# Kernel optimization log

Hardware: AMD Instinct MI355X
Metric: run time of the kernel (lower is better)

The kernel has to match this reference:

```python
import jax, jax.numpy as jnp
import numpy as np

B, T, C, H = 32, 1024, 384, 64

def setup_inputs() -> dict:
    key = jax.random.key(0)
    k1, k2, k3, k4 = jax.random.split(key, 4)
    x = jax.random.normal(k1, (B, T, C), dtype=jnp.float32)
    s = 1.0 / np.sqrt(C)
    Wk = jax.random.normal(k2, (C, H), dtype=jnp.float32) * s
    Wq = jax.random.normal(k3, (C, H), dtype=jnp.float32) * s
    Wv = jax.random.normal(k4, (C, H), dtype=jnp.float32) * s
    return {"x": x, "Wk": Wk, "Wq": Wq, "Wv": Wv}

def reference(x, Wk, Wq, Wv):
    # Single-head causal attention (dropout = identity, eval mode).
    Tn = x.shape[1]
    k = jnp.einsum('btc,ch->bth', x, Wk)   # [B,T,H]
    q = jnp.einsum('btc,ch->bth', x, Wq)
    v = jnp.einsum('btc,ch->bth', x, Wv)
    scale = k.shape[-1] ** -0.5
    wei = jnp.einsum('bth,bsh->bts', q, k) * scale  # [B,T,T]
    causal = jnp.tril(jnp.ones((Tn, Tn), dtype=bool))
    wei = jnp.where(causal, wei, -jnp.inf)
    wei = jax.nn.softmax(wei, axis=-1)
    out = jnp.einsum('bts,bsh->bth', wei, v)  # [B,T,H]
    return out
```

## Files before the change

kernel.cpp:

```cpp
#include <hip/hip_runtime.h>

#define BB 32
#define TT 1024
#define CCH 384
#define HH 64

typedef short short8 __attribute__((ext_vector_type(8)));
typedef float f32x4 __attribute__((ext_vector_type(4)));
typedef unsigned short ushort;

static __device__ __forceinline__ ushort f2bf(float f) {
    union { float f; unsigned u; } v; v.f = f;
    unsigned r = v.u + 0x7fff + ((v.u >> 16) & 1);
    return (ushort)(r >> 16);
}

__global__ void wswz(const float* __restrict__ Wk, const float* __restrict__ Wq,
                     const float* __restrict__ Wv, ushort* __restrict__ wf) {
    const int mat = blockIdx.x, ks = blockIdx.y;
    const float* W = (mat == 0) ? Wk : ((mat == 1) ? Wq : Wv);
    const int t = threadIdx.x;
    const int ct = t >> 6, lane = t & 63, quad = lane >> 4, l15 = lane & 15;
    const int col = ct * 16 + l15;
    short8 d;
#pragma unroll
    for (int j = 0; j < 8; ++j)
        d[j] = (short)f2bf(W[(ks * 32 + quad * 8 + j) * 64 + col]);
    *(short8*)(wf + (((mat * 12 + ks) * 4 + ct) << 9) + lane * 8) = d;
}

#define XSTR 388
#define VS_STRIDE 68

__global__ __launch_bounds__(256, 2) void qkv(const float* __restrict__ x,
                                              const ushort* __restrict__ wf,
                                              ushort* __restrict__ kb,
                                              ushort* __restrict__ qb,
                                              ushort* __restrict__ vtb) {
    const int r0 = blockIdx.x * 64;
    const int tid = threadIdx.x;
    const int wv = tid >> 6, lane = tid & 63, l15 = lane & 15, quad = lane >> 4;

    __shared__ ushort xs[64 * XSTR];

#pragma unroll
    for (int kb3 = 0; kb3 < 3; ++kb3) {
        const int kbase = kb3 * 128;
        const int seg = (tid & 7) * 16;
#pragma unroll
        for (int i = 0; i < 2; ++i) {
            const int r = (tid >> 3) + 32 * i;
            const float* src = x + (size_t)(r0 + r) * CCH + kbase + seg;
            f32x4 v0 = *(const f32x4*)(src);
            f32x4 v1 = *(const f32x4*)(src + 4);
            f32x4 v2 = *(const f32x4*)(src + 8);
            f32x4 v3 = *(const f32x4*)(src + 12);
            short8 p0, p1;
#pragma unroll
            for (int j = 0; j < 4; ++j) {
                p0[j]     = (short)f2bf(v0[j]);
                p0[j + 4] = (short)f2bf(v1[j]);
                p1[j]     = (short)f2bf(v2[j]);
                p1[j + 4] = (short)f2bf(v3[j]);
            }
            *(short8*)(xs + r * XSTR + kbase + seg) = p0;
            *(short8*)(xs + r * XSTR + kbase + seg + 8) = p1;
        }
    }
    __syncthreads();

    f32x4 acc[12] = {};
    short8 bf[2][12];
#pragma unroll
    for (int m = 0; m < 3; ++m)
#pragma unroll
        for (int ct = 0; ct < 4; ++ct)
            bf[0][m * 4 + ct] = *(const short8*)(wf + (((m * 12 + 0) * 4 + ct) << 9) + lane * 8);

#pragma unroll
    for (int ks = 0; ks < 12; ++ks) {
        short8 a = *(const short8*)(xs + (wv * 16 + l15) * XSTR + ks * 32 + quad * 8);
        if (ks < 11) {
#pragma unroll
            for (int m = 0; m < 3; ++m)
#pragma unroll
                for (int ct = 0; ct < 4; ++ct)
                    bf[(ks + 1) & 1][m * 4 + ct] =
                        *(const short8*)(wf + (((m * 12 + ks + 1) * 4 + ct) << 9) + lane * 8);
        }
#pragma unroll
        for (int f = 0; f < 12; ++f)
            acc[f] = __builtin_amdgcn_mfma_f32_16x16x32_bf16(a, bf[ks & 1][f], acc[f], 0, 0, 0);
    }

#pragma unroll
    for (int ct = 0; ct < 4; ++ct) {
#pragma unroll
        for (int r = 0; r < 4; ++r) {
            int row = r0 + wv * 16 + quad * 4 + r;
            int col = ct * 16 + l15;
            kb[row * 64 + col] = f2bf(acc[0 + ct][r]);
            qb[row * 64 + col] = f2bf(acc[4 + ct][r]);
        }
    }
    __syncthreads();
    ushort* vs = xs;
#pragma unroll
    for (int ct = 0; ct < 4; ++ct)
#pragma unroll
        for (int r = 0; r < 4; ++r)
            vs[(wv * 16 + quad * 4 + r) * VS_STRIDE + ct * 16 + l15] = f2bf(acc[8 + ct][r]);
    __syncthreads();
    {
        const int col = tid >> 2;
        const int rbase = (tid & 3) * 16;
        short8 d0, d1;
#pragma unroll
        for (int j = 0; j < 8; ++j) {
            d0[j] = (short)vs[(rbase + j) * VS_STRIDE + col];
            d1[j] = (short)vs[(rbase + 8 + j) * VS_STRIDE + col];
        }
        const int b = r0 >> 10;
        const int t = (r0 & 1023) + rbase;
        *(short8*)(vtb + b * 65536 + col * 1024 + t) = d0;
        *(short8*)(vtb + b * 65536 + col * 1024 + t + 8) = d1;
    }
}

#define PSTR2 40
#define KSTR 72
#define VSTR 136

__global__ __launch_bounds__(256, 3) void attn(const ushort* __restrict__ qb,
                                               const ushort* __restrict__ kb,
                                               const ushort* __restrict__ vtb,
                                               float* __restrict__ out) {
    const int y = blockIdx.y;
    int qt;
    if (y < 8)       qt = 31 - y;
    else if (y < 16) qt = y - 8;
    else if (y < 24) qt = 39 - y;
    else             qt = y - 16;
    const int b = blockIdx.x;
    const int t0 = qt * 32;
    const int tid = threadIdx.x;
    const int w = tid >> 6, lane = tid & 63, l15 = lane & 15, quad = lane >> 4;

    __shared__ __align__(16) char arena[46080];
    ushort* Ks = (ushort*)arena;
    ushort* Vs = (ushort*)(arena + 18432);
    ushort* Ps = (ushort*)(arena + 35840);
    ushort* Psw = Ps + w * 32 * PSTR2;

    const ushort* kbb = kb  + (size_t)b * 65536;
    const ushort* vbb = vtb + (size_t)b * 65536;

    short8 qf0[2], qf1[2];
#pragma unroll
    for (int m = 0; m < 2; ++m) {
        const int qrow = b * 1024 + t0 + m * 16 + l15;
        qf0[m] = *(const short8*)(qb + qrow * 64 + quad * 8);
        qf1[m] = *(const short8*)(qb + qrow * 64 + 32 + quad * 8);
    }

    f32x4 o[2][4] = {};
    float li[2][4] = {};
    const float c1 = 0.125f * 1.4426950408889634f;
    const float c2 = 10.0f * 1.4426950408889634f;

    const int nst = (qt >> 2) + 1;

    short8 kr[4], vr[4];
#pragma unroll
    for (int i = 0; i < 4; ++i) {
        int c = tid + i * 256;
        kr[i] = *(const short8*)(kbb + (c >> 3) * 64 + (c & 7) * 8);
        vr[i] = *(const short8*)(vbb + (c >> 4) * 1024 + (c & 15) * 8);
    }

    for (int it = 0; it < nst; ++it) {
        const int s0 = it * 128;
        __syncthreads();
#pragma unroll
        for (int i = 0; i < 4; ++i) {
            int c = tid + i * 256;
            *(short8*)(Ks + (c >> 3) * KSTR + (c & 7) * 8) = kr[i];
            *(short8*)(Vs + (c >> 4) * VSTR + (c & 15) * 8) = vr[i];
        }
        __syncthreads();
        if (it + 1 < nst) {
            const int sn = s0 + 128;
#pragma unroll
            for (int i = 0; i < 4; ++i) {
                int c = tid + i * 256;
                kr[i] = *(const short8*)(kbb + (sn + (c >> 3)) * 64 + (c & 7) * 8);
                vr[i] = *(const short8*)(vbb + (c >> 4) * 1024 + sn + (c & 15) * 8);
            }
        }

        f32x4 s[2][2];
        __builtin_amdgcn_s_setprio(1);
#pragma unroll
        for (int g = 0; g < 2; ++g) {
            const ushort* kp = Ks + (w * 32 + g * 16 + l15) * KSTR + quad * 8;
            short8 b0 = *(const short8*)(kp);
            short8 b1 = *(const short8*)(kp + 32);
#pragma unroll
            for (int m = 0; m < 2; ++m) {
                f32x4 z = {};
                z = __builtin_amdgcn_mfma_f32_16x16x32_bf16(qf0[m], b0, z, 0, 0, 0);
                s[m][g] = __builtin_amdgcn_mfma_f32_16x16x32_bf16(qf1[m], b1, z, 0, 0, 0);
            }
        }
        __builtin_amdgcn_s_setprio(0);

        if (it + 1 < nst) {
#pragma unroll
            for (int m = 0; m < 2; ++m)
#pragma unroll
                for (int g = 0; g < 2; ++g)
#pragma unroll
                    for (int r = 0; r < 4; ++r) {
                        float p = exp2f(s[m][g][r] * c1 - c2);
                        li[m][r] += p;
                        Psw[(m * 16 + quad * 4 + r) * PSTR2 + g * 16 + l15] = f2bf(p);
                    }
        } else {
#pragma unroll
            for (int m = 0; m < 2; ++m)
#pragma unroll
                for (int g = 0; g < 2; ++g)
#pragma unroll
                    for (int r = 0; r < 4; ++r) {
                        const int trow = t0 + m * 16 + quad * 4 + r;
                        const int col = s0 + w * 32 + g * 16 + l15;
                        float p = (col <= trow) ? exp2f(s[m][g][r] * c1 - c2) : 0.f;
                        li[m][r] += p;
                        Psw[(m * 16 + quad * 4 + r) * PSTR2 + g * 16 + l15] = f2bf(p);
                    }
        }

        short8 pa[2];
#pragma unroll
        for (int m = 0; m < 2; ++m)
            pa[m] = *(const short8*)(Psw + (m * 16 + l15) * PSTR2 + quad * 8);

        __builtin_amdgcn_s_setprio(1);
        short8 vbf[4];
#pragma unroll
        for (int ct = 0; ct < 4; ++ct)
            vbf[ct] = *(const short8*)(Vs + (ct * 16 + l15) * VSTR + w * 32 + quad * 8);
#pragma unroll
        for (int m = 0; m < 2; ++m)
#pragma unroll
            for (int ct = 0; ct < 4; ++ct)
                o[m][ct] = __builtin_amdgcn_mfma_f32_16x16x32_bf16(pa[m], vbf[ct], o[m][ct], 0, 0, 0);
        __builtin_amdgcn_s_setprio(0);
    }

    __syncthreads();

#pragma unroll
    for (int m = 0; m < 2; ++m)
#pragma unroll
        for (int r = 0; r < 4; ++r) {
            float rs = li[m][r];
#pragma unroll
            for (int off = 1; off < 16; off <<= 1)
                rs += __shfl_xor(rs, off);
            li[m][r] = rs;
        }

    float* slotO = (float*)arena;
    float* slotL = (float*)(arena + 34816);
#pragma unroll
    for (int m = 0; m < 2; ++m) {
        const int sl = w * 2 + m;
#pragma unroll
        for (int ct = 0; ct < 4; ++ct)
#pragma unroll
            for (int r = 0; r < 4; ++r)
                slotO[(sl * 4 + ct) * 272 + (quad * 4 + r) * 17 + l15] = o[m][ct][r];
        if (l15 == 0)
#pragma unroll
            for (int r = 0; r < 4; ++r)
                slotL[sl * 16 + quad * 4 + r] = li[m][r];
    }
    __syncthreads();

    {
        const int mh = w >> 1, cb = (w & 1) * 2;
#pragma unroll
        for (int r = 0; r < 4; ++r) {
            float lsum = 0.f;
#pragma unroll
            for (int wp = 0; wp < 4; ++wp)
                lsum += slotL[(wp * 2 + mh) * 16 + quad * 4 + r];
            const float inv = 1.0f / lsum;
            const int t = t0 + mh * 16 + quad * 4 + r;
#pragma unroll
            for (int cc = 0; cc < 2; ++cc) {
                const int ct = cb + cc;
                float v = 0.f;
#pragma unroll
                for (int wp = 0; wp < 4; ++wp)
                    v += slotO[((wp * 2 + mh) * 4 + ct) * 272 + (quad * 4 + r) * 17 + l15];
                out[b * 65536 + t * 64 + ct * 16 + l15] = v * inv;
            }
        }
    }
}

extern "C" void kernel_launch(void* const* d_in, const int* in_sizes, int n_in,
                              void* d_out, int out_size, void* d_ws, size_t ws_size,
                              hipStream_t stream) {
    const float* x  = (const float*)d_in[0];
    const float* Wk = (const float*)d_in[1];
    const float* Wq = (const float*)d_in[2];
    const float* Wv = (const float*)d_in[3];

    char* ws = (char*)d_ws;
    ushort* wf  = (ushort*)ws;
    ushort* kb  = (ushort*)(ws + 256 * 1024);
    ushort* qb  = (ushort*)(ws + 256 * 1024 + 4u * 1024 * 1024);
    ushort* vtb = (ushort*)(ws + 256 * 1024 + 8u * 1024 * 1024);

    wswz<<<dim3(3, 12), dim3(256), 0, stream>>>(Wk, Wq, Wv, wf);
    qkv<<<dim3(512), dim3(256), 0, stream>>>(x, wf, kb, qb, vtb);
    attn<<<dim3(32, 32), dim3(256), 0, stream>>>(qb, kb, vtb, (float*)d_out);
}
```

Before: 121.0 us.

## Fuse QKV projection and attention into one kernel with per-batch semaphores

Merges the QKV projection and attention kernels into one persistent 512-block kernel. Each block first projects 64 rows, then waits on a per-batch atomic counter until all 16 blocks of that batch finish. It then computes attention for a paired heavy/light query tile so causal work is balanced, sharing K/V tile loads between the two tiles. This removes a kernel launch and the tail imbalance, but depends on all 512 blocks being co-resident (spin-wait deadlock risk) and raises register pressure.

```diff
diff --git a/kernel.cpp b/kernel.cpp
--- a/kernel.cpp
+++ b/kernel.cpp
@@ -16,8 +16,10 @@
 }
 
 __global__ void wswz(const float* __restrict__ Wk, const float* __restrict__ Wq,
-                     const float* __restrict__ Wv, ushort* __restrict__ wf) {
+                     const float* __restrict__ Wv, ushort* __restrict__ wf,
+                     unsigned* __restrict__ sem) {
     const int mat = blockIdx.x, ks = blockIdx.y;
+    if (mat == 0 && ks == 0 && threadIdx.x < 32) sem[threadIdx.x] = 0u;
     const float* W = (mat == 0) ? Wk : ((mat == 1) ? Wq : Wv);
     const int t = threadIdx.x;
     const int ct = t >> 6, lane = t & 63, quad = lane >> 4, l15 = lane & 15;
@@ -31,232 +33,15 @@
 
 #define XSTR 388
 #define VS_STRIDE 68
-
-__global__ __launch_bounds__(256, 2) void qkv(const float* __restrict__ x,
-                                              const ushort* __restrict__ wf,
-                                              ushort* __restrict__ kb,
-                                              ushort* __restrict__ qb,
-                                              ushort* __restrict__ vtb) {
-    const int r0 = blockIdx.x * 64;
-    const int tid = threadIdx.x;
-    const int wv = tid >> 6, lane = tid & 63, l15 = lane & 15, quad = lane >> 4;
-
-    __shared__ ushort xs[64 * XSTR];
-
-#pragma unroll
-    for (int kb3 = 0; kb3 < 3; ++kb3) {
-        const int kbase = kb3 * 128;
-        const int seg = (tid & 7) * 16;
-#pragma unroll
-        for (int i = 0; i < 2; ++i) {
-            const int r = (tid >> 3) + 32 * i;
-            const float* src = x + (size_t)(r0 + r) * CCH + kbase + seg;
-            f32x4 v0 = *(const f32x4*)(src);
-            f32x4 v1 = *(const f32x4*)(src + 4);
-            f32x4 v2 = *(const f32x4*)(src + 8);
-            f32x4 v3 = *(const f32x4*)(src + 12);
-            short8 p0, p1;
-#pragma unroll
-            for (int j = 0; j < 4; ++j) {
-                p0[j]     = (short)f2bf(v0[j]);
-                p0[j + 4] = (short)f2bf(v1[j]);
-                p1[j]     = (short)f2bf(v2[j]);
-                p1[j + 4] = (short)f2bf(v3[j]);
-            }
-            *(short8*)(xs + r * XSTR + kbase + seg) = p0;
-            *(short8*)(xs + r * XSTR + kbase + seg + 8) = p1;
-        }
-    }
-    __syncthreads();
-
-    f32x4 acc[12] = {};
-    short8 bf[2][12];
-#pragma unroll
-    for (int m = 0; m < 3; ++m)
-#pragma unroll
-        for (int ct = 0; ct < 4; ++ct)
-            bf[0][m * 4 + ct] = *(const short8*)(wf + (((m * 12 + 0) * 4 + ct) << 9) + lane * 8);
-
-#pragma unroll
-    for (int ks = 0; ks < 12; ++ks) {
-        short8 a = *(const short8*)(xs + (wv * 16 + l15) * XSTR + ks * 32 + quad * 8);
-        if (ks < 11) {
-#pragma unroll
-            for (int m = 0; m < 3; ++m)
-#pragma unroll
-                for (int ct = 0; ct < 4; ++ct)
-                    bf[(ks + 1) & 1][m * 4 + ct] =
-                        *(const short8*)(wf + (((m * 12 + ks + 1) * 4 + ct) << 9) + lane * 8);
-        }
-#pragma unroll
-        for (int f = 0; f < 12; ++f)
-            acc[f] = __builtin_amdgcn_mfma_f32_16x16x32_bf16(a, bf[ks & 1][f], acc[f], 0, 0, 0);
-    }
-
-#pragma unroll
-    for (int ct = 0; ct < 4; ++ct) {
-#pragma unroll
-        for (int r = 0; r < 4; ++r) {
-            int row = r0 + wv * 16 + quad * 4 + r;
-            int col = ct * 16 + l15;
-            kb[row * 64 + col] = f2bf(acc[0 + ct][r]);
-            qb[row * 64 + col] = f2bf(acc[4 + ct][r]);
-        }
-    }
-    __syncthreads();
-    ushort* vs = xs;
-#pragma unroll
-    for (int ct = 0; ct < 4; ++ct)
-#pragma unroll
-        for (int r = 0; r < 4; ++r)
-            vs[(wv * 16 + quad * 4 + r) * VS_STRIDE + ct * 16 + l15] = f2bf(acc[8 + ct][r]);
-    __syncthreads();
-    {
-        const int col = tid >> 2;
-        const int rbase = (tid & 3) * 16;
-        short8 d0, d1;
-#pragma unroll
-        for (int j = 0; j < 8; ++j) {
-            d0[j] = (short)vs[(rbase + j) * VS_STRIDE + col];
-            d1[j] = (short)vs[(rbase + 8 + j) * VS_STRIDE + col];
-        }
-        const int b = r0 >> 10;
-        const int t = (r0 & 1023) + rbase;
-        *(short8*)(vtb + b * 65536 + col * 1024 + t) = d0;
-        *(short8*)(vtb + b * 65536 + col * 1024 + t + 8) = d1;
-    }
-}
-
 #define PSTR2 40
 #define KSTR 72
 #define VSTR 136
 
-__global__ __launch_bounds__(256, 3) void attn(const ushort* __restrict__ qb,
-                                               const ushort* __restrict__ kb,
-                                               const ushort* __restrict__ vtb,
-                                               float* __restrict__ out) {
-    const int y = blockIdx.y;
-    int qt;
-    if (y < 8)       qt = 31 - y;
-    else if (y < 16) qt = y - 8;
-    else if (y < 24) qt = 39 - y;
-    else             qt = y - 16;
-    const int b = blockIdx.x;
-    const int t0 = qt * 32;
-    const int tid = threadIdx.x;
-    const int w = tid >> 6, lane = tid & 63, l15 = lane & 15, quad = lane >> 4;
-
-    __shared__ __align__(16) char arena[46080];
-    ushort* Ks = (ushort*)arena;
-    ushort* Vs = (ushort*)(arena + 18432);
-    ushort* Ps = (ushort*)(arena + 35840);
-    ushort* Psw = Ps + w * 32 * PSTR2;
-
-    const ushort* kbb = kb  + (size_t)b * 65536;
-    const ushort* vbb = vtb + (size_t)b * 65536;
-
-    short8 qf0[2], qf1[2];
-#pragma unroll
-    for (int m = 0; m < 2; ++m) {
-        const int qrow = b * 1024 + t0 + m * 16 + l15;
-        qf0[m] = *(const short8*)(qb + qrow * 64 + quad * 8);
-        qf1[m] = *(const short8*)(qb + qrow * 64 + 32 + quad * 8);
-    }
-
-    f32x4 o[2][4] = {};
-    float li[2][4] = {};
-    const float c1 = 0.125f * 1.4426950408889634f;
-    const float c2 = 10.0f * 1.4426950408889634f;
-
-    const int nst = (qt >> 2) + 1;
-
-    short8 kr[4], vr[4];
-#pragma unroll
-    for (int i = 0; i < 4; ++i) {
-        int c = tid + i * 256;
-        kr[i] = *(const short8*)(kbb + (c >> 3) * 64 + (c & 7) * 8);
-        vr[i] = *(const short8*)(vbb + (c >> 4) * 1024 + (c & 15) * 8);
-    }
-
-    for (int it = 0; it < nst; ++it) {
-        const int s0 = it * 128;
-        __syncthreads();
-#pragma unroll
-        for (int i = 0; i < 4; ++i) {
-            int c = tid + i * 256;
-            *(short8*)(Ks + (c >> 3) * KSTR + (c & 7) * 8) = kr[i];
-            *(short8*)(Vs + (c >> 4) * VSTR + (c & 15) * 8) = vr[i];
-        }
-        __syncthreads();
-        if (it + 1 < nst) {
-            const int sn = s0 + 128;
-#pragma unroll
-            for (int i = 0; i < 4; ++i) {
-                int c = tid + i * 256;
-                kr[i] = *(const short8*)(kbb + (sn + (c >> 3)) * 64 + (c & 7) * 8);
-                vr[i] = *(const short8*)(vbb + (c >> 4) * 1024 + sn + (c & 15) * 8);
-            }
-        }
-
-        f32x4 s[2][2];
-        __builtin_amdgcn_s_setprio(1);
-#pragma unroll
-        for (int g = 0; g < 2; ++g) {
-            const ushort* kp = Ks + (w * 32 + g * 16 + l15) * KSTR + quad * 8;
-            short8 b0 = *(const short8*)(kp);
-            short8 b1 = *(const short8*)(kp + 32);
-#pragma unroll
-            for (int m = 0; m < 2; ++m) {
-                f32x4 z = {};
-                z = __builtin_amdgcn_mfma_f32_16x16x32_bf16(qf0[m], b0, z, 0, 0, 0);
-                s[m][g] = __builtin_amdgcn_mfma_f32_16x16x32_bf16(qf1[m], b1, z, 0, 0, 0);
-            }
-        }
-        __builtin_amdgcn_s_setprio(0);
-
-        if (it + 1 < nst) {
-#pragma unroll
-            for (int m = 0; m < 2; ++m)
-#pragma unroll
-                for (int g = 0; g < 2; ++g)
-#pragma unroll
-                    for (int r = 0; r < 4; ++r) {
-                        float p = exp2f(s[m][g][r] * c1 - c2);
-                        li[m][r] += p;
-                        Psw[(m * 16 + quad * 4 + r) * PSTR2 + g * 16 + l15] = f2bf(p);
-                    }
-        } else {
-#pragma unroll
-            for (int m = 0; m < 2; ++m)
-#pragma unroll
-                for (int g = 0; g < 2; ++g)
-#pragma unroll
-                    for (int r = 0; r < 4; ++r) {
-                        const int trow = t0 + m * 16 + quad * 4 + r;
-                        const int col = s0 + w * 32 + g * 16 + l15;
-                        float p = (col <= trow) ? exp2f(s[m][g][r] * c1 - c2) : 0.f;
-                        li[m][r] += p;
-                        Psw[(m * 16 + quad * 4 + r) * PSTR2 + g * 16 + l15] = f2bf(p);
-                    }
-        }
-
-        short8 pa[2];
-#pragma unroll
-        for (int m = 0; m < 2; ++m)
-            pa[m] = *(const short8*)(Psw + (m * 16 + l15) * PSTR2 + quad * 8);
-
-        __builtin_amdgcn_s_setprio(1);
-        short8 vbf[4];
-#pragma unroll
-        for (int ct = 0; ct < 4; ++ct)
-            vbf[ct] = *(const short8*)(Vs + (ct * 16 + l15) * VSTR + w * 32 + quad * 8);
-#pragma unroll
-        for (int m = 0; m < 2; ++m)
-#pragma unroll
-            for (int ct = 0; ct < 4; ++ct)
-                o[m][ct] = __builtin_amdgcn_mfma_f32_16x16x32_bf16(pa[m], vbf[ct], o[m][ct], 0, 0, 0);
-        __builtin_amdgcn_s_setprio(0);
-    }
+static __device__ __forceinline__ void attn_epilogue(
+    char* arena, f32x4 (&o)[2][4], float (&li)[2][4],
+    int w, int quad, int l15, int t0, int b, float* __restrict__ out) {
+    float* slotO = (float*)arena;
+    float* slotL = (float*)(arena + 34816);
 
     __syncthreads();
 
@@ -271,8 +56,6 @@
             li[m][r] = rs;
         }
 
-    float* slotO = (float*)arena;
-    float* slotL = (float*)(arena + 34816);
 #pragma unroll
     for (int m = 0; m < 2; ++m) {
         const int sl = w * 2 + m;
@@ -288,26 +71,318 @@
     }
     __syncthreads();
 
+    const int mh = w >> 1, cb = (w & 1) * 2;
+#pragma unroll
+    for (int r = 0; r < 4; ++r) {
+        float lsum = 0.f;
+#pragma unroll
+        for (int wp = 0; wp < 4; ++wp)
+            lsum += slotL[(wp * 2 + mh) * 16 + quad * 4 + r];
+        const float inv = 1.0f / lsum;
+        const int t = t0 + mh * 16 + quad * 4 + r;
+#pragma unroll
+        for (int cc = 0; cc < 2; ++cc) {
+            const int ct = cb + cc;
+            float v = 0.f;
+#pragma unroll
+            for (int wp = 0; wp < 4; ++wp)
+                v += slotO[((wp * 2 + mh) * 4 + ct) * 272 + (quad * 4 + r) * 17 + l15];
+            out[b * 65536 + t * 64 + ct * 16 + l15] = v * inv;
+        }
+    }
+}
+
+__global__ __launch_bounds__(256, 2) void qkattn(const float* __restrict__ x,
+                                                 const ushort* __restrict__ wf,
+                                                 ushort* __restrict__ kb,
+                                                 ushort* __restrict__ qb,
+                                                 ushort* __restrict__ vtb,
+                                                 float* __restrict__ out,
+                                                 unsigned* __restrict__ sem) {
+    __shared__ __align__(16) char arena[49664];
+
+    const int gb = blockIdx.x;
+    const int tid = threadIdx.x;
+    const int w = tid >> 6, lane = tid & 63, l15 = lane & 15, quad = lane >> 4;
+    const int beta = gb >> 4, sB = gb & 15;
+
     {
-        const int mh = w >> 1, cb = (w & 1) * 2;
-#pragma unroll
-        for (int r = 0; r < 4; ++r) {
-            float lsum = 0.f;
-#pragma unroll
-            for (int wp = 0; wp < 4; ++wp)
-                lsum += slotL[(wp * 2 + mh) * 16 + quad * 4 + r];
-            const float inv = 1.0f / lsum;
-            const int t = t0 + mh * 16 + quad * 4 + r;
-#pragma unroll
-            for (int cc = 0; cc < 2; ++cc) {
-                const int ct = cb + cc;
-                float v = 0.f;
-#pragma unroll
-                for (int wp = 0; wp < 4; ++wp)
-                    v += slotO[((wp * 2 + mh) * 4 + ct) * 272 + (quad * 4 + r) * 17 + l15];
-                out[b * 65536 + t * 64 + ct * 16 + l15] = v * inv;
-            }
-        }
+        const int r0 = gb * 64;
+        ushort* xs = (ushort*)arena;
+
+#pragma unroll
+        for (int kb3 = 0; kb3 < 3; ++kb3) {
+            const int kbase = kb3 * 128;
+            const int seg = (tid & 7) * 16;
+#pragma unroll
+            for (int i = 0; i < 2; ++i) {
+                const int r = (tid >> 3) + 32 * i;
+                const float* src = x + (size_t)(r0 + r) * CCH + kbase + seg;
+                f32x4 v0 = *(const f32x4*)(src);
+                f32x4 v1 = *(const f32x4*)(src + 4);
+                f32x4 v2 = *(const f32x4*)(src + 8);
+                f32x4 v3 = *(const f32x4*)(src + 12);
+                short8 p0, p1;
+#pragma unroll
+                for (int j = 0; j < 4; ++j) {
+                    p0[j]     = (short)f2bf(v0[j]);
+                    p0[j + 4] = (short)f2bf(v1[j]);
+                    p1[j]     = (short)f2bf(v2[j]);
+                    p1[j + 4] = (short)f2bf(v3[j]);
+                }
+                *(short8*)(xs + r * XSTR + kbase + seg) = p0;
+                *(short8*)(xs + r * XSTR + kbase + seg + 8) = p1;
+            }
+        }
+        __syncthreads();
+
+        f32x4 acc[12] = {};
+        short8 bfrag[2][12];
+#pragma unroll
+        for (int m = 0; m < 3; ++m)
+#pragma unroll
+            for (int ct = 0; ct < 4; ++ct)
+                bfrag[0][m * 4 + ct] = *(const short8*)(wf + (((m * 12 + 0) * 4 + ct) << 9) + lane * 8);
+
+#pragma unroll
+        for (int ks = 0; ks < 12; ++ks) {
+            short8 a = *(const short8*)(xs + (w * 16 + l15) * XSTR + ks * 32 + quad * 8);
+            if (ks < 11) {
+#pragma unroll
+                for (int m = 0; m < 3; ++m)
+#pragma unroll
+                    for (int ct = 0; ct < 4; ++ct)
+                        bfrag[(ks + 1) & 1][m * 4 + ct] =
+                            *(const short8*)(wf + (((m * 12 + ks + 1) * 4 + ct) << 9) + lane * 8);
+            }
+#pragma unroll
+            for (int f = 0; f < 12; ++f)
+                acc[f] = __builtin_amdgcn_mfma_f32_16x16x32_bf16(a, bfrag[ks & 1][f], acc[f], 0, 0, 0);
+        }
+
+#pragma unroll
+        for (int ct = 0; ct < 4; ++ct) {
+#pragma unroll
+            for (int r = 0; r < 4; ++r) {
+                int row = r0 + w * 16 + quad * 4 + r;
+                int col = ct * 16 + l15;
+                kb[row * 64 + col] = f2bf(acc[0 + ct][r]);
+                qb[row * 64 + col] = f2bf(acc[4 + ct][r]);
+            }
+        }
+        __syncthreads();
+        ushort* vs = xs;
+#pragma unroll
+        for (int ct = 0; ct < 4; ++ct)
+#pragma unroll
+            for (int r = 0; r < 4; ++r)
+                vs[(w * 16 + quad * 4 + r) * VS_STRIDE + ct * 16 + l15] = f2bf(acc[8 + ct][r]);
+        __syncthreads();
+        {
+            const int col = tid >> 2;
+            const int rbase = (tid & 3) * 16;
+            short8 d0, d1;
+#pragma unroll
+            for (int j = 0; j < 8; ++j) {
+                d0[j] = (short)vs[(rbase + j) * VS_STRIDE + col];
+                d1[j] = (short)vs[(rbase + 8 + j) * VS_STRIDE + col];
+            }
+            const int bq = r0 >> 10;
+            const int t = (r0 & 1023) + rbase;
+            *(short8*)(vtb + bq * 65536 + col * 1024 + t) = d0;
+            *(short8*)(vtb + bq * 65536 + col * 1024 + t + 8) = d1;
+        }
+    }
+
+    __threadfence();
+    __syncthreads();
+    if (tid == 0) {
+        __hip_atomic_fetch_add(&sem[beta], 1u, __ATOMIC_RELEASE, __HIP_MEMORY_SCOPE_AGENT);
+        while (__hip_atomic_load(&sem[beta], __ATOMIC_ACQUIRE, __HIP_MEMORY_SCOPE_AGENT) < 16u)
+            __builtin_amdgcn_s_sleep(8);
+    }
+    __syncthreads();
+
+    {
+        const int b = beta;
+        const int qtH = 16 + sB, qtL = 15 - sB;
+        const int t0H = qtH * 32, t0L = qtL * 32;
+        const int nstH = (qtH >> 2) + 1;
+        const int nstL = (qtL >> 2) + 1;
+
+        ushort* Ks = (ushort*)arena;
+        ushort* Vs = (ushort*)(arena + 18432);
+        ushort* Ps = (ushort*)(arena + 35840);
+        ushort* Psw = Ps + w * 32 * PSTR2;
+
+        const ushort* kbb = kb  + (size_t)b * 65536;
+        const ushort* vbb = vtb + (size_t)b * 65536;
+
+        short8 qf0H[2], qf1H[2], qf0L[2], qf1L[2];
+#pragma unroll
+        for (int m = 0; m < 2; ++m) {
+            const int qrH = b * 1024 + t0H + m * 16 + l15;
+            qf0H[m] = *(const short8*)(qb + qrH * 64 + quad * 8);
+            qf1H[m] = *(const short8*)(qb + qrH * 64 + 32 + quad * 8);
+            const int qrL = b * 1024 + t0L + m * 16 + l15;
+            qf0L[m] = *(const short8*)(qb + qrL * 64 + quad * 8);
+            qf1L[m] = *(const short8*)(qb + qrL * 64 + 32 + quad * 8);
+        }
+
+        f32x4 oH[2][4] = {}, oL[2][4] = {};
+        float liH[2][4] = {}, liL[2][4] = {};
+        const float c1 = 0.125f * 1.4426950408889634f;
+        const float c2 = 10.0f * 1.4426950408889634f;
+
+        short8 kr[4], vr[4];
+#pragma unroll
+        for (int i = 0; i < 4; ++i) {
+            int c = tid + i * 256;
+            kr[i] = *(const short8*)(kbb + (c >> 3) * 64 + (c & 7) * 8);
+            vr[i] = *(const short8*)(vbb + (c >> 4) * 1024 + (c & 15) * 8);
+        }
+
+        for (int it = 0; it < nstH; ++it) {
+            const int s0 = it * 128;
+            __syncthreads();
+#pragma unroll
+            for (int i = 0; i < 4; ++i) {
+                int c = tid + i * 256;
+                *(short8*)(Ks + (c >> 3) * KSTR + (c & 7) * 8) = kr[i];
+                *(short8*)(Vs + (c >> 4) * VSTR + (c & 15) * 8) = vr[i];
+            }
+            __syncthreads();
+            if (it + 1 < nstH) {
+                const int sn = s0 + 128;
+#pragma unroll
+                for (int i = 0; i < 4; ++i) {
+                    int c = tid + i * 256;
+                    kr[i] = *(const short8*)(kbb + (sn + (c >> 3)) * 64 + (c & 7) * 8);
+                    vr[i] = *(const short8*)(vbb + (c >> 4) * 1024 + sn + (c & 15) * 8);
+                }
+            }
+
+            short8 kb0[2], kb1[2];
+#pragma unroll
+            for (int g = 0; g < 2; ++g) {
+                const ushort* kp = Ks + (w * 32 + g * 16 + l15) * KSTR + quad * 8;
+                kb0[g] = *(const short8*)(kp);
+                kb1[g] = *(const short8*)(kp + 32);
+            }
+            short8 vbf[4];
+#pragma unroll
+            for (int ct = 0; ct < 4; ++ct)
+                vbf[ct] = *(const short8*)(Vs + (ct * 16 + l15) * VSTR + w * 32 + quad * 8);
+
+            {
+                f32x4 s[2][2];
+                __builtin_amdgcn_s_setprio(1);
+#pragma unroll
+                for (int g = 0; g < 2; ++g)
+#pragma unroll
+                    for (int m = 0; m < 2; ++m) {
+                        f32x4 z = {};
+                        z = __builtin_amdgcn_mfma_f32_16x16x32_bf16(qf0H[m], kb0[g], z, 0, 0, 0);
+                        s[m][g] = __builtin_amdgcn_mfma_f32_16x16x32_bf16(qf1H[m], kb1[g], z, 0, 0, 0);
+                    }
+                __builtin_amdgcn_s_setprio(0);
+
+                if (it + 1 < nstH) {
+#pragma unroll
+                    for (int m = 0; m < 2; ++m)
+#pragma unroll
+                        for (int g = 0; g < 2; ++g)
+#pragma unroll
+                            for (int r = 0; r < 4; ++r) {
+                                float p = exp2f(s[m][g][r] * c1 - c2);
+                                liH[m][r] += p;
+                                Psw[(m * 16 + quad * 4 + r) * PSTR2 + g * 16 + l15] = f2bf(p);
+                            }
+                } else {
+#pragma unroll
+                    for (int m = 0; m < 2; ++m)
+#pragma unroll
+                        for (int g = 0; g < 2; ++g)
+#pragma unroll
+                            for (int r = 0; r < 4; ++r) {
+                                const int trow = t0H + m * 16 + quad * 4 + r;
+                                const int col = s0 + w * 32 + g * 16 + l15;
+                                float p = (col <= trow) ? exp2f(s[m][g][r] * c1 - c2) : 0.f;
+                                liH[m][r] += p;
+                                Psw[(m * 16 + quad * 4 + r) * PSTR2 + g * 16 + l15] = f2bf(p);
+                            }
+                }
+
+                short8 pa[2];
+#pragma unroll
+                for (int m = 0; m < 2; ++m)
+                    pa[m] = *(const short8*)(Psw + (m * 16 + l15) * PSTR2 + quad * 8);
+
+                __builtin_amdgcn_s_setprio(1);
+#pragma unroll
+                for (int m = 0; m < 2; ++m)
+#pragma unroll
+                    for (int ct = 0; ct < 4; ++ct)
+                        oH[m][ct] = __builtin_amdgcn_mfma_f32_16x16x32_bf16(pa[m], vbf[ct], oH[m][ct], 0, 0, 0);
+                __builtin_amdgcn_s_setprio(0);
+            }
+
+            if (it < nstL) {
+                f32x4 s[2][2];
+                __builtin_amdgcn_s_setprio(1);
+#pragma unroll
+                for (int g = 0; g < 2; ++g)
+#pragma unroll
+                    for (int m = 0; m < 2; ++m) {
+                        f32x4 z = {};
+                        z = __builtin_amdgcn_mfma_f32_16x16x32_bf16(qf0L[m], kb0[g], z, 0, 0, 0);
+                        s[m][g] = __builtin_amdgcn_mfma_f32_16x16x32_bf16(qf1L[m], kb1[g], z, 0, 0, 0);
+                    }
+                __builtin_amdgcn_s_setprio(0);
+
+                if (it + 1 < nstL) {
+#pragma unroll
+                    for (int m = 0; m < 2; ++m)
+#pragma unroll
+                        for (int g = 0; g < 2; ++g)
+#pragma unroll
+                            for (int r = 0; r < 4; ++r) {
+                                float p = exp2f(s[m][g][r] * c1 - c2);
+                                liL[m][r] += p;
+                                Psw[(m * 16 + quad * 4 + r) * PSTR2 + g * 16 + l15] = f2bf(p);
+                            }
+                } else {
+#pragma unroll
+                    for (int m = 0; m < 2; ++m)
+#pragma unroll
+                        for (int g = 0; g < 2; ++g)
+#pragma unroll
+                            for (int r = 0; r < 4; ++r) {
+                                const int trow = t0L + m * 16 + quad * 4 + r;
+                                const int col = s0 + w * 32 + g * 16 + l15;
+                                float p = (col <= trow) ? exp2f(s[m][g][r] * c1 - c2) : 0.f;
+                                liL[m][r] += p;
+                                Psw[(m * 16 + quad * 4 + r) * PSTR2 + g * 16 + l15] = f2bf(p);
+                            }
+                }
+
+                short8 pa[2];
+#pragma unroll
+                for (int m = 0; m < 2; ++m)
+                    pa[m] = *(const short8*)(Psw + (m * 16 + l15) * PSTR2 + quad * 8);
+
+                __builtin_amdgcn_s_setprio(1);
+#pragma unroll
+                for (int m = 0; m < 2; ++m)
+#pragma unroll
+                    for (int ct = 0; ct < 4; ++ct)
+                        oL[m][ct] = __builtin_amdgcn_mfma_f32_16x16x32_bf16(pa[m], vbf[ct], oL[m][ct], 0, 0, 0);
+                __builtin_amdgcn_s_setprio(0);
+            }
+        }
+
+        attn_epilogue(arena, oH, liH, w, quad, l15, t0H, b, out);
+        attn_epilogue(arena, oL, liL, w, quad, l15, t0L, b, out);
     }
 }
 
@@ -321,11 +396,11 @@
 
     char* ws = (char*)d_ws;
     ushort* wf  = (ushort*)ws;
+    unsigned* sem = (unsigned*)(ws + 200 * 1024);
     ushort* kb  = (ushort*)(ws + 256 * 1024);
     ushort* qb  = (ushort*)(ws + 256 * 1024 + 4u * 1024 * 1024);
     ushort* vtb = (ushort*)(ws + 256 * 1024 + 8u * 1024 * 1024);
 
-    wswz<<<dim3(3, 12), dim3(256), 0, stream>>>(Wk, Wq, Wv, wf);
-    qkv<<<dim3(512), dim3(256), 0, stream>>>(x, wf, kb, qb, vtb);
-    attn<<<dim3(32, 32), dim3(256), 0, stream>>>(qb, kb, vtb, (float*)d_out);
+    wswz<<<dim3(3, 12), dim3(256), 0, stream>>>(Wk, Wq, Wv, wf, sem);
+    qkattn<<<dim3(512), dim3(256), 0, stream>>>(x, wf, kb, qb, vtb, (float*)d_out, sem);
 }
```

Measured after the change: 220.6 us. 82.2% more time.
